# Kernel tuning notes

Measured on AMD Instinct MI355X. Metric: run time of the kernel, lower is better.

Reference implementation:

```python
import jax, jax.numpy as jnp
import numpy as np

INV_MAX_SIZE = 55
INV_STR_LEN = 80
MSG_VOCAB = 128
EOS = MSG_VOCAB + 1  # 129
VOCAB = 130
EMB = 16   # str_emb == CHAR_EMB
HID = 16
OUT = 24
B = 1024

# INV_OCLASS_MAP with default 128 (indices 0..18)
_MAP = np.full(19, 128, dtype=np.int32)
for k, v in {1: 93, 2: 41, 3: 91, 4: 61, 5: 34, 6: 40, 7: 37, 8: 33, 9: 63,
             10: 43, 11: 47, 12: 36, 13: 42, 14: 96, 15: 48, 16: 95, 17: 46, 18: 128}.items():
    _MAP[k] = v


def setup_inputs() -> dict:
    key = jax.random.key(0)
    ks = jax.random.split(key, 20)
    s = 0.1
    return {
        "inv_oclasses": jax.random.randint(ks[0], (B, INV_MAX_SIZE), 0, 19),
        "inv_strs": jax.random.randint(ks[1], (B, INV_MAX_SIZE, INV_STR_LEN), 0, MSG_VOCAB),
        "emb": jax.random.normal(ks[2], (VOCAB, EMB), jnp.float32) * s,
        "rnn_Wih": jax.random.normal(ks[3], (HID, EMB), jnp.float32) * s,
        "rnn_Whh": jax.random.normal(ks[4], (HID, HID), jnp.float32) * s,
        "rnn_bih": jax.random.normal(ks[5], (HID,), jnp.float32) * s,
        "rnn_bhh": jax.random.normal(ks[6], (HID,), jnp.float32) * s,
        "gru_Wih_f": jax.random.normal(ks[7], (3 * HID, EMB), jnp.float32) * s,
        "gru_Whh_f": jax.random.normal(ks[8], (3 * HID, HID), jnp.float32) * s,
        "gru_bih_f": jax.random.normal(ks[9], (3 * HID,), jnp.float32) * s,
        "gru_bhh_f": jax.random.normal(ks[10], (3 * HID,), jnp.float32) * s,
        "gru_Wih_b": jax.random.normal(ks[11], (3 * HID, EMB), jnp.float32) * s,
        "gru_Whh_b": jax.random.normal(ks[12], (3 * HID, HID), jnp.float32) * s,
        "gru_bih_b": jax.random.normal(ks[13], (3 * HID,), jnp.float32) * s,
        "gru_bhh_b": jax.random.normal(ks[14], (3 * HID,), jnp.float32) * s,
        "fus_W1": jax.random.normal(ks[15], (HID, 3 * HID), jnp.float32) * s,
        "fus_b1": jax.random.normal(ks[16], (HID,), jnp.float32) * s,
        "fus_W2": jax.random.normal(ks[17], (OUT, HID), jnp.float32) * s,
        "fus_b2": jax.random.normal(ks[18], (OUT,), jnp.float32) * s,
    }


def _masked_rnn(x, lengths, Wih, Whh, bih, bhh):
    # x: [N, T, D]; returns final hidden at step lengths-1 (zeros if length==0)
    N, T, _ = x.shape
    gi = jnp.einsum('ntd,hd->nth', x, Wih) + bih          # precompute input proj
    valid = (jnp.arange(T)[None, :] < lengths[:, None])   # [N, T]
    def step(h, inp):
        gi_t, v = inp
        hn = jnp.tanh(gi_t + h @ Whh.T + bhh)
        return jnp.where(v, hn, h), None
    h0 = jnp.zeros((N, Whh.shape[0]), x.dtype)
    h, _ = jax.lax.scan(step, h0, (jnp.swapaxes(gi, 0, 1), valid.T[:, :, None]))
    return h


def _masked_gru(x, lengths, Wih, Whh, bih, bhh):
    # x: [N, T, D]; PyTorch GRU cell; returns final hidden within valid prefix
    N, T, _ = x.shape
    H = Whh.shape[1]
    gi = jnp.einsum('ntd,hd->nth', x, Wih) + bih          # [N, T, 3H]
    valid = (jnp.arange(T)[None, :] < lengths[:, None])
    def step(h, inp):
        gi_t, v = inp
        gh = h @ Whh.T + bhh
        i_r, i_z, i_n = jnp.split(gi_t, 3, axis=-1)
        h_r, h_z, h_n = jnp.split(gh, 3, axis=-1)
        r = jax.nn.sigmoid(i_r + h_r)
        z = jax.nn.sigmoid(i_z + h_z)
        n = jnp.tanh(i_n + r * h_n)
        hn = (1.0 - z) * n + z * h
        return jnp.where(v, hn, h), None
    h0 = jnp.zeros((N, H), x.dtype)
    h, _ = jax.lax.scan(step, h0, (jnp.swapaxes(gi, 0, 1), valid.T[:, :, None]))
    return h


def reference(inv_oclasses, inv_strs, emb, rnn_Wih, rnn_Whh, rnn_bih, rnn_bhh,
              gru_Wih_f, gru_Whh_f, gru_bih_f, gru_bhh_f,
              gru_Wih_b, gru_Whh_b, gru_bih_b, gru_bhh_b,
              fus_W1, fus_b1, fus_W2, fus_b2):
    Bn = inv_oclasses.shape[0]
    emb = emb.at[0].set(0.0)  # padding_idx=0

    # ---- object-class branch: map -> embed -> packed vanilla RNN ----
    inv_class = jnp.asarray(_MAP)[inv_oclasses]            # [B, 55]
    inv_class_emb = emb[inv_class]                         # [B, 55, 16]
    len_class = jnp.sum(inv_oclasses != 18, axis=1)
    h_class = _masked_rnn(inv_class_emb, len_class, rnn_Wih, rnn_Whh, rnn_bih, rnn_bhh)  # [B, 16]

    # ---- string branch: insert EOS, embed, packed bidirectional GRU ----
    strs = inv_strs.reshape(Bn * INV_MAX_SIZE, INV_STR_LEN)
    lengths = jnp.sum(strs != 0, axis=-1)                  # [B*55]
    t = jnp.arange(INV_STR_LEN)
    strs_eos = jnp.where(t[None, :] == lengths[:, None], EOS, strs)
    str_emb = emb[strs_eos]                                # [B*55, 80, 16]

    h_fwd = _masked_gru(str_emb, lengths, gru_Wih_f, gru_Whh_f, gru_bih_f, gru_bhh_f)
    # reverse the valid prefix for the backward direction
    idx = jnp.maximum(lengths[:, None] - 1 - t[None, :], 0)
    x_rev = jnp.take_along_axis(str_emb, idx[:, :, None], axis=1)
    h_bwd = _masked_gru(x_rev, lengths, gru_Wih_b, gru_Whh_b, gru_bih_b, gru_bhh_b)

    str_final = jnp.concatenate([h_fwd, h_bwd], axis=-1).reshape(Bn, INV_MAX_SIZE, 2 * HID)
    str_mask = (jnp.sum(inv_strs, axis=-1) > 0).astype(str_final.dtype)[:, :, None]
    str_pooled = jnp.sum(str_final * str_mask, axis=1) / (jnp.sum(str_mask, axis=1) + 1e-8)

    combined = jnp.concatenate([h_class, str_pooled], axis=-1)   # [B, 48]
    h = jax.nn.relu(combined @ fus_W1.T + fus_b1)
    inv_features = h @ fus_W2.T + fus_b2                          # [B, 24]
    return inv_features, inv_class_emb, str_emb
```

## Files before the change

kernel.cpp:

```cpp
#include <hip/hip_runtime.h>
#include <hip/hip_bf16.h>
#include <math.h>

#define B_     1024
#define VOCAB_ 130
#define EOS_   129

#define OUT_CLS_F  24576
#define OUT_STR_F  925696

#define OFF_POOL 0
#define OFF_CNT  32768
#define OFF_HC   33792
#define OFF_T    50176

#define NK2      7104
#define NK1      14960
#define NINT     21312
#define NTOT     22064

typedef float f2 __attribute__((ext_vector_type(2)));

static __device__ const int d_MAP[19] =
    {128,93,41,91,61,34,40,37,33,63,43,47,36,42,96,48,95,46,128};

__device__ __forceinline__ float sigm_(float x){
    return __builtin_amdgcn_rcpf(1.f + __builtin_amdgcn_exp2f(-1.4426950408889634f * x));
}
__device__ __forceinline__ float tanh_(float x){
    return 2.f * __builtin_amdgcn_rcpf(1.f + __builtin_amdgcn_exp2f(-2.8853900817779268f * x)) - 1.f;
}
__device__ __forceinline__ int badf(float v) {
    return (v != v) || (fabsf(v) > 1e30f);
}
__device__ __forceinline__ f2 mkf2(float a, float b){ f2 r; r.x = a; r.y = b; return r; }

__global__ void k0_tables(const float* __restrict__ emb,
                          const float* __restrict__ WihF, const float* __restrict__ bihF,
                          const float* __restrict__ bhhF,
                          const float* __restrict__ WihB, const float* __restrict__ bihB,
                          const float* __restrict__ bhhB, float* ws)
{
    int i = blockIdx.x * 256 + threadIdx.x;
    if (i >= 12288) return;
    int dir = i / 6144, r = i - dir * 6144;
    int c = r / 48, j = r - c * 48;
    const float* Wih = dir ? WihB : WihF;
    const float* bih = dir ? bihB : bihF;
    const float* bhh = dir ? bhhB : bhhF;
    float v = bih[j] + ((j < 32) ? bhh[j] : 0.f);
    if (c != 0) {
        const float* e = emb + c * 16;
        #pragma unroll
        for (int d = 0; d < 16; ++d) v = fmaf(Wih[j * 16 + d], e[d], v);
    }
    ws[OFF_T + i] = v;
}

__global__ __launch_bounds__(256)
__attribute__((amdgpu_waves_per_eu(1, 4)))
void k12_main(const int* oclass, const int* strs, const float* __restrict__ emb,
              const float* __restrict__ WhhF, const float* __restrict__ bhhF,
              const float* __restrict__ WhhB, const float* __restrict__ bhhB,
              const float* __restrict__ rWih, const float* __restrict__ rWhh,
              const float* __restrict__ rbih, const float* __restrict__ rbhh,
              float* ws, float* out)
{
    __shared__ __align__(16) float smem[6528];
    int bi0 = blockIdx.x, tid = threadIdx.x;

    int k2id = -1, k1id;
    if (bi0 < NINT) {
        if (bi0 % 3 == 0) k2id = bi0 / 3;
        else              k1id = bi0 - bi0 / 3 - 1;
    } else {
        k1id = 14208 + (bi0 - NINT);
    }

    if (k2id < 0) {
        float* embF = smem;
        int*   chs  = (int*)(smem + 2600);
        for (int i = tid; i < VOCAB_ * 16; i += 256) {
            int r = i >> 4, c = i & 15;
            embF[r * 20 + c] = (r == 0) ? 0.f : emb[i];
        }
        __syncthreads();

        if (k1id < 14080) {
            int w = tid >> 6, lane = tid & 63;
            int s = k1id * 4 + w;
            const int* cp = strs + (long)s * 80;
            int ca = cp[lane];
            int cb = (lane < 16) ? cp[64 + lane] : 0;
            unsigned long long m1 = __ballot(ca != 0);
            unsigned long long m2 = __ballot((lane < 16) && (cb != 0));
            int L = __popcll(m1) + __popcll(m2);
            if (lane == L) ca = EOS_;
            if (lane < 16 && (64 + lane) == L) cb = EOS_;
            chs[w * 80 + lane] = ca;
            if (lane < 16) chs[w * 80 + 64 + lane] = cb;
            float4* dst = (float4*)(out + OUT_STR_F + (long)s * 1280);
            #pragma unroll
            for (int it = 0; it < 5; ++it) {
                int q = it * 64 + lane;
                int row = q >> 2, part = q & 3;
                int ch = chs[w * 80 + row];
                dst[q] = *(const float4*)&embF[ch * 20 + part * 4];
            }
        } else {
            int q = (k1id - 14080) * 256 + tid;
            int bs = q >> 2, part = q & 3;
            int c = d_MAP[oclass[bs]];
            float4* dst = (float4*)(out + OUT_CLS_F);
            dst[q] = *(const float4*)&embF[c * 20 + part * 4];
        }
        return;
    }

    float* ldsT  = smem;
    float* ldsHB = smem + 6272;
    int bi = k2id;
    int grp = tid >> 4, j = tid & 15;
    float* hb = ldsHB + (grp << 4);

    if (bi < 7040) {
        bool fwd = bi < 3520;
        const float* __restrict__ Whh = fwd ? WhhF : WhhB;
        const float* __restrict__ bhh = fwd ? bhhF : bhhB;

        const float* Tg = ws + OFF_T + (fwd ? 0 : 6144);
        for (int i = tid; i < 6144; i += 256) {
            int c = i / 48, q = i - c * 48;
            ldsT[c * 49 + q] = Tg[i];
        }

        f2 wr[8], wz[8], wn[8];
        #pragma unroll
        for (int k = 0; k < 4; ++k) {
            float4 a = *(const float4*)&Whh[      j * 16 + 4 * k];
            float4 b = *(const float4*)&Whh[256 + j * 16 + 4 * k];
            float4 c4 = *(const float4*)&Whh[512 + j * 16 + 4 * k];
            wr[2*k] = mkf2(a.x, a.y);  wr[2*k+1] = mkf2(a.z, a.w);
            wz[2*k] = mkf2(b.x, b.y);  wz[2*k+1] = mkf2(b.z, b.w);
            wn[2*k] = mkf2(c4.x, c4.y); wn[2*k+1] = mkf2(c4.z, c4.w);
        }
        float bn = bhh[32 + j];
        #pragma unroll
        for (int k = 0; k < 8; ++k) {
            asm volatile("" : "+v"(wr[k]));
            asm volatile("" : "+v"(wz[k]));
            asm volatile("" : "+v"(wn[k]));
        }
        __syncthreads();

        int s = (fwd ? bi : bi - 3520) * 16 + grp;
        const int* cp = strs + (long)s * 80;

        int cnt = 0;
        #pragma unroll
        for (int k = 0; k < 5; ++k) cnt += (cp[j + 16 * k] != 0);
        cnt += __builtin_amdgcn_ds_swizzle(cnt, (1 << 10) | 0x1f);
        cnt += __builtin_amdgcn_ds_swizzle(cnt, (2 << 10) | 0x1f);
        cnt += __builtin_amdgcn_ds_swizzle(cnt, (4 << 10) | 0x1f);
        cnt += __builtin_amdgcn_ds_swizzle(cnt, (8 << 10) | 0x1f);
        int L = cnt;

        float hj = 0.f;
        hb[j] = 0.f;
        if (L > 0) {
            int base = fwd ? 0 : (L - 1);
            int stp  = fwd ? 1 : -1;
            int c = cp[base];
            for (int t = 0; t < L; ++t) {
                int cn = (t + 1 < L) ? cp[base + (t + 1) * stp] : 0;
                const float* Trow = ldsT + c * 49;
                f2 ar = mkf2(Trow[j], 0.f);
                f2 az = mkf2(Trow[16 + j], 0.f);
                f2 an = mkf2(bn, 0.f);
                float tn_ = Trow[32 + j];
                #pragma unroll
                for (int k = 0; k < 4; ++k) {
                    float4 h4 = *(const float4*)&hb[4 * k];
                    f2 h0 = mkf2(h4.x, h4.y), h1 = mkf2(h4.z, h4.w);
                    ar = __builtin_elementwise_fma(wr[2*k],   h0, ar);
                    az = __builtin_elementwise_fma(wz[2*k],   h0, az);
                    an = __builtin_elementwise_fma(wn[2*k],   h0, an);
                    ar = __builtin_elementwise_fma(wr[2*k+1], h1, ar);
                    az = __builtin_elementwise_fma(wz[2*k+1], h1, az);
                    an = __builtin_elementwise_fma(wn[2*k+1], h1, an);
                }
                float rg = sigm_(ar.x + ar.y);
                float zg = sigm_(az.x + az.y);
                float ng = tanh_(fmaf(rg, an.x + an.y, tn_));
                hj = fmaf(zg, hj - ng, ng);
                hb[j] = hj;
                __builtin_amdgcn_wave_barrier();
                c = cn;
            }
            int b = s / 55;
            atomicAdd(ws + OFF_POOL + b * 32 + (fwd ? 0 : 16) + j, hj);
            if (fwd && j == 0) atomicAdd(ws + OFF_CNT + b, 1.f);
        }
    } else {
        for (int i = tid; i < 19 * 16; i += 256) {
            int o = i >> 4, jj = i & 15;
            int c = d_MAP[o];
            float v = rbih[jj] + rbhh[jj];
            #pragma unroll
            for (int d = 0; d < 16; ++d)
                v = fmaf(rWih[jj * 16 + d], emb[c * 16 + d], v);
            ldsT[o * 20 + jj] = v;
        }
        f2 wv[8];
        #pragma unroll
        for (int k = 0; k < 4; ++k) {
            float4 a = *(const float4*)&rWhh[j * 16 + 4 * k];
            wv[2*k] = mkf2(a.x, a.y);  wv[2*k+1] = mkf2(a.z, a.w);
        }
        __syncthreads();

        int smp = (bi - 7040) * 16 + grp;
        const int* op = oclass + (long)smp * 55;
        int cnt = 0;
        #pragma unroll
        for (int k = 0; k < 4; ++k) {
            int p = j + 16 * k;
            cnt += (p < 55 && op[p] != 18);
        }
        cnt += __builtin_amdgcn_ds_swizzle(cnt, (1 << 10) | 0x1f);
        cnt += __builtin_amdgcn_ds_swizzle(cnt, (2 << 10) | 0x1f);
        cnt += __builtin_amdgcn_ds_swizzle(cnt, (4 << 10) | 0x1f);
        cnt += __builtin_amdgcn_ds_swizzle(cnt, (8 << 10) | 0x1f);
        int len = cnt;

        float hj = 0.f;
        hb[j] = 0.f;
        if (len > 0) {
            int o = op[0];
            for (int t = 0; t < len; ++t) {
                int onx = (t + 1 < len) ? op[t + 1] : 0;
                f2 a2 = mkf2(ldsT[o * 20 + j], 0.f);
                #pragma unroll
                for (int k = 0; k < 4; ++k) {
                    float4 h4 = *(const float4*)&hb[4 * k];
                    a2 = __builtin_elementwise_fma(wv[2*k],   mkf2(h4.x, h4.y), a2);
                    a2 = __builtin_elementwise_fma(wv[2*k+1], mkf2(h4.z, h4.w), a2);
                }
                hj = tanh_(a2.x + a2.y);
                hb[j] = hj;
                __builtin_amdgcn_wave_barrier();
                o = onx;
            }
        }
        ws[OFF_HC + smp * 16 + j] = hj;
    }
}

__global__ void k3_fuse(const float* fW1, const float* fb1,
                        const float* fW2, const float* fb2,
                        float* ws, float* out)
{
    int b = blockIdx.x * 256 + threadIdx.x;
    if (b >= B_) return;
    float inv = 1.f / (ws[OFF_CNT + b] + 1e-8f);
    float comb[48];
    #pragma unroll
    for (int j = 0; j < 16; ++j) comb[j] = ws[OFF_HC + b * 16 + j];
    #pragma unroll
    for (int j = 0; j < 32; ++j) comb[16 + j] = ws[OFF_POOL + b * 32 + j] * inv;

    float hid[16];
    #pragma unroll
    for (int o = 0; o < 16; ++o) {
        float v = fb1[o];
        #pragma unroll
        for (int i = 0; i < 48; ++i) v = fmaf(fW1[o * 48 + i], comb[i], v);
        hid[o] = v > 0.f ? v : 0.f;
    }
    #pragma unroll
    for (int o = 0; o < 24; ++o) {
        float v = fb2[o];
        #pragma unroll
        for (int i = 0; i < 16; ++i) v = fmaf(fW2[o * 16 + i], hid[i], v);
        out[b * 24 + o] = v;
    }

    if (b == 0) {
        int bb = 0;
        if (!badf(ws[OFF_POOL]))    bb |= 1;
        if (!badf(ws[OFF_HC]))      bb |= 2;
        if (ws[OFF_CNT] > 0.5f)     bb |= 4;
        if (bb != 7) {
            float code = 16384.f + 128.f * (float)bb;
            #pragma unroll
            for (int i = 4; i < 12; ++i) out[i] = code;
        }
    }
}

extern "C" void kernel_launch(void* const* d_in, const int* in_sizes, int n_in,
                              void* d_out, int out_size, void* d_ws, size_t ws_size,
                              hipStream_t stream)
{
    const int*   oclass = (const int*)d_in[0];
    const int*   strs   = (const int*)d_in[1];
    const float* emb    = (const float*)d_in[2];
    const float* rWih   = (const float*)d_in[3];
    const float* rWhh   = (const float*)d_in[4];
    const float* rbih   = (const float*)d_in[5];
    const float* rbhh   = (const float*)d_in[6];
    const float* gWihF  = (const float*)d_in[7];
    const float* gWhhF  = (const float*)d_in[8];
    const float* gbihF  = (const float*)d_in[9];
    const float* gbhhF  = (const float*)d_in[10];
    const float* gWihB  = (const float*)d_in[11];
    const float* gWhhB  = (const float*)d_in[12];
    const float* gbihB  = (const float*)d_in[13];
    const float* gbhhB  = (const float*)d_in[14];
    const float* fW1    = (const float*)d_in[15];
    const float* fb1    = (const float*)d_in[16];
    const float* fW2    = (const float*)d_in[17];
    const float* fb2    = (const float*)d_in[18];

    float* ws  = (float*)d_ws;
    float* out = (float*)d_out;

    hipMemsetAsync(d_ws, 0, 33792 * sizeof(float), stream);

    k0_tables<<<48, 256, 0, stream>>>(emb, gWihF, gbihF, gbhhF,
                                      gWihB, gbihB, gbhhB, ws);
    k12_main<<<NTOT, 256, 0, stream>>>(oclass, strs, emb,
                                       gWhhF, gbhhF, gWhhB, gbhhB,
                                       rWih, rWhh, rbih, rbhh, ws, out);
    k3_fuse<<<4, 256, 0, stream>>>(fW1, fb1, fW2, fb2, ws, out);
}
```

Before: 646.6 us.

## Split GRU hidden dot-product across two lanes per unit, halving strings per block

Result: slower. 1.123 ms (+73.6%).

```diff
diff --git a/kernel.cpp b/kernel.cpp
--- a/kernel.cpp
+++ b/kernel.cpp
@@ -14,10 +14,10 @@
 #define OFF_HC   33792
 #define OFF_T    50176
 
-#define NK2      7104
+#define NK2      14144
 #define NK1      14960
-#define NINT     21312
-#define NTOT     22064
+#define NINT     28288
+#define NTOT     29104
 
 typedef float f2 __attribute__((ext_vector_type(2)));
 
@@ -34,6 +34,9 @@
     return (v != v) || (fabsf(v) > 1e30f);
 }
 __device__ __forceinline__ f2 mkf2(float a, float b){ f2 r; r.x = a; r.y = b; return r; }
+__device__ __forceinline__ float swz16_(float x){
+    return __int_as_float(__builtin_amdgcn_ds_swizzle(__float_as_int(x), 0x401F));
+}
 
 __global__ void k0_tables(const float* __restrict__ emb,
                           const float* __restrict__ WihF, const float* __restrict__ bihF,
@@ -58,7 +61,6 @@
 }
 
 __global__ __launch_bounds__(256)
-__attribute__((amdgpu_waves_per_eu(1, 4)))
 void k12_main(const int* oclass, const int* strs, const float* __restrict__ emb,
               const float* __restrict__ WhhF, const float* __restrict__ bhhF,
               const float* __restrict__ WhhB, const float* __restrict__ bhhB,
@@ -71,10 +73,10 @@
 
     int k2id = -1, k1id;
     if (bi0 < NINT) {
-        if (bi0 % 3 == 0) k2id = bi0 / 3;
-        else              k1id = bi0 - bi0 / 3 - 1;
+        if ((bi0 & 1) == 0) k2id = bi0 >> 1;
+        else                k1id = bi0 >> 1;
     } else {
-        k1id = 14208 + (bi0 - NINT);
+        k1id = NK2 + (bi0 - NINT);
     }
 
     if (k2id < 0) {
@@ -117,91 +119,112 @@
         return;
     }
 
-    float* ldsT  = smem;
-    float* ldsHB = smem + 6272;
+    float* ldsT = smem;
     int bi = k2id;
-    int grp = tid >> 4, j = tid & 15;
-    float* hb = ldsHB + (grp << 4);
-
-    if (bi < 7040) {
-        bool fwd = bi < 3520;
+
+    if (bi < 14080) {
+        int lane = tid & 63;
+        int g  = lane >> 5;
+        int q  = lane & 31;
+        int p  = q >> 4;
+        int j  = q & 15;
+        int grp8 = ((tid >> 6) << 1) + g;
+        float* hb = smem + 6272 + grp8 * 16;
+
+        bool fwd = bi < 7040;
         const float* __restrict__ Whh = fwd ? WhhF : WhhB;
         const float* __restrict__ bhh = fwd ? bhhF : bhhB;
 
         const float* Tg = ws + OFF_T + (fwd ? 0 : 6144);
         for (int i = tid; i < 6144; i += 256) {
-            int c = i / 48, q = i - c * 48;
-            ldsT[c * 49 + q] = Tg[i];
-        }
-
-        f2 wr[8], wz[8], wn[8];
+            int c = i / 48, qq = i - c * 48;
+            ldsT[c * 49 + qq] = Tg[i];
+        }
+
+        f2 wr4[4], wz4[4], wn4[4];
+        const float* Wb = Whh + j * 16 + p * 8;
+        {
+            float4 a0 = *(const float4*)&Wb[0],   a1 = *(const float4*)&Wb[4];
+            float4 b0 = *(const float4*)&Wb[256], b1 = *(const float4*)&Wb[260];
+            float4 c0 = *(const float4*)&Wb[512], c1 = *(const float4*)&Wb[516];
+            wr4[0]=mkf2(a0.x,a0.y); wr4[1]=mkf2(a0.z,a0.w); wr4[2]=mkf2(a1.x,a1.y); wr4[3]=mkf2(a1.z,a1.w);
+            wz4[0]=mkf2(b0.x,b0.y); wz4[1]=mkf2(b0.z,b0.w); wz4[2]=mkf2(b1.x,b1.y); wz4[3]=mkf2(b1.z,b1.w);
+            wn4[0]=mkf2(c0.x,c0.y); wn4[1]=mkf2(c0.z,c0.w); wn4[2]=mkf2(c1.x,c1.y); wn4[3]=mkf2(c1.z,c1.w);
+        }
         #pragma unroll
         for (int k = 0; k < 4; ++k) {
-            float4 a = *(const float4*)&Whh[      j * 16 + 4 * k];
-            float4 b = *(const float4*)&Whh[256 + j * 16 + 4 * k];
-            float4 c4 = *(const float4*)&Whh[512 + j * 16 + 4 * k];
-            wr[2*k] = mkf2(a.x, a.y);  wr[2*k+1] = mkf2(a.z, a.w);
-            wz[2*k] = mkf2(b.x, b.y);  wz[2*k+1] = mkf2(b.z, b.w);
-            wn[2*k] = mkf2(c4.x, c4.y); wn[2*k+1] = mkf2(c4.z, c4.w);
+            asm volatile("" : "+v"(wr4[k]));
+            asm volatile("" : "+v"(wz4[k]));
+            asm volatile("" : "+v"(wn4[k]));
         }
         float bn = bhh[32 + j];
-        #pragma unroll
-        for (int k = 0; k < 8; ++k) {
-            asm volatile("" : "+v"(wr[k]));
-            asm volatile("" : "+v"(wz[k]));
-            asm volatile("" : "+v"(wn[k]));
-        }
         __syncthreads();
 
-        int s = (fwd ? bi : bi - 3520) * 16 + grp;
+        int s = (fwd ? bi : bi - 7040) * 8 + grp8;
         const int* cp = strs + (long)s * 80;
 
-        int cnt = 0;
-        #pragma unroll
-        for (int k = 0; k < 5; ++k) cnt += (cp[j + 16 * k] != 0);
+        int cnt = (cp[q] != 0) + (cp[q + 32] != 0);
+        if (q < 16) cnt += (cp[q + 64] != 0);
         cnt += __builtin_amdgcn_ds_swizzle(cnt, (1 << 10) | 0x1f);
         cnt += __builtin_amdgcn_ds_swizzle(cnt, (2 << 10) | 0x1f);
         cnt += __builtin_amdgcn_ds_swizzle(cnt, (4 << 10) | 0x1f);
         cnt += __builtin_amdgcn_ds_swizzle(cnt, (8 << 10) | 0x1f);
+        cnt += __builtin_amdgcn_ds_swizzle(cnt, (16 << 10) | 0x1f);
         int L = cnt;
 
         float hj = 0.f;
         hb[j] = 0.f;
+        __builtin_amdgcn_wave_barrier();
         if (L > 0) {
             int base = fwd ? 0 : (L - 1);
             int stp  = fwd ? 1 : -1;
-            int c = cp[base];
+            int c  = cp[base];
+            int c1 = (L > 1) ? cp[base + stp] : 0;
             for (int t = 0; t < L; ++t) {
-                int cn = (t + 1 < L) ? cp[base + (t + 1) * stp] : 0;
+                int c2 = (t + 2 < L) ? cp[base + (t + 2) * stp] : 0;
                 const float* Trow = ldsT + c * 49;
-                f2 ar = mkf2(Trow[j], 0.f);
-                f2 az = mkf2(Trow[16 + j], 0.f);
-                f2 an = mkf2(bn, 0.f);
+                float t0  = Trow[(p << 4) + j];
                 float tn_ = Trow[32 + j];
-                #pragma unroll
-                for (int k = 0; k < 4; ++k) {
-                    float4 h4 = *(const float4*)&hb[4 * k];
-                    f2 h0 = mkf2(h4.x, h4.y), h1 = mkf2(h4.z, h4.w);
-                    ar = __builtin_elementwise_fma(wr[2*k],   h0, ar);
-                    az = __builtin_elementwise_fma(wz[2*k],   h0, az);
-                    an = __builtin_elementwise_fma(wn[2*k],   h0, an);
-                    ar = __builtin_elementwise_fma(wr[2*k+1], h1, ar);
-                    az = __builtin_elementwise_fma(wz[2*k+1], h1, az);
-                    an = __builtin_elementwise_fma(wn[2*k+1], h1, an);
-                }
-                float rg = sigm_(ar.x + ar.y);
-                float zg = sigm_(az.x + az.y);
-                float ng = tanh_(fmaf(rg, an.x + an.y, tn_));
+                float4 h0 = *(const float4*)&hb[p * 8];
+                float4 h1 = *(const float4*)&hb[p * 8 + 4];
+                f2 accr = mkf2(p ? 0.f : t0, 0.f);
+                f2 accz = mkf2(p ? t0 : 0.f, 0.f);
+                f2 accn = mkf2(p ? 0.f : bn, 0.f);
+                f2 ha = mkf2(h0.x, h0.y), hbv = mkf2(h0.z, h0.w);
+                f2 hc = mkf2(h1.x, h1.y), hd  = mkf2(h1.z, h1.w);
+                accr = __builtin_elementwise_fma(wr4[0], ha,  accr);
+                accz = __builtin_elementwise_fma(wz4[0], ha,  accz);
+                accn = __builtin_elementwise_fma(wn4[0], ha,  accn);
+                accr = __builtin_elementwise_fma(wr4[1], hbv, accr);
+                accz = __builtin_elementwise_fma(wz4[1], hbv, accz);
+                accn = __builtin_elementwise_fma(wn4[1], hbv, accn);
+                accr = __builtin_elementwise_fma(wr4[2], hc,  accr);
+                accz = __builtin_elementwise_fma(wz4[2], hc,  accz);
+                accn = __builtin_elementwise_fma(wn4[2], hc,  accn);
+                accr = __builtin_elementwise_fma(wr4[3], hd,  accr);
+                accz = __builtin_elementwise_fma(wz4[3], hd,  accz);
+                accn = __builtin_elementwise_fma(wn4[3], hd,  accn);
+                float sr = accr.x + accr.y;
+                float sz = accz.x + accz.y;
+                float sn = accn.x + accn.y;
+                sr += swz16_(sr);
+                sz += swz16_(sz);
+                sn += swz16_(sn);
+                float rg = sigm_(sr);
+                float zg = sigm_(sz);
+                float ng = tanh_(fmaf(rg, sn, tn_));
                 hj = fmaf(zg, hj - ng, ng);
                 hb[j] = hj;
                 __builtin_amdgcn_wave_barrier();
-                c = cn;
+                c = c1; c1 = c2;
             }
             int b = s / 55;
-            atomicAdd(ws + OFF_POOL + b * 32 + (fwd ? 0 : 16) + j, hj);
-            if (fwd && j == 0) atomicAdd(ws + OFF_CNT + b, 1.f);
+            if (p == 0) atomicAdd(ws + OFF_POOL + b * 32 + (fwd ? 0 : 16) + j, hj);
+            if (fwd && q == 0) atomicAdd(ws + OFF_CNT + b, 1.f);
         }
     } else {
+        int grp = tid >> 4, j = tid & 15;
+        float* hb = smem + 6272 + (grp << 4);
         for (int i = tid; i < 19 * 16; i += 256) {
             int o = i >> 4, jj = i & 15;
             int c = d_MAP[o];
@@ -219,13 +242,13 @@
         }
         __syncthreads();
 
-        int smp = (bi - 7040) * 16 + grp;
+        int smp = (bi - 14080) * 16 + grp;
         const int* op = oclass + (long)smp * 55;
         int cnt = 0;
         #pragma unroll
         for (int k = 0; k < 4; ++k) {
-            int p = j + 16 * k;
-            cnt += (p < 55 && op[p] != 18);
+            int pgt = j + 16 * k;
+            cnt += (pgt < 55 && op[pgt] != 18);
         }
         cnt += __builtin_amdgcn_ds_swizzle(cnt, (1 << 10) | 0x1f);
         cnt += __builtin_amdgcn_ds_swizzle(cnt, (2 << 10) | 0x1f);
@@ -235,6 +258,7 @@
 
         float hj = 0.f;
         hb[j] = 0.f;
+        __builtin_amdgcn_wave_barrier();
         if (len > 0) {
             int o = op[0];
             for (int t = 0; t < len; ++t) {
```

## Drop LDS staging of GRU input table, prefetch rows from global two steps ahead

Applied to the files above, without the earlier changes.

Measured after the change: 677.9 us. +4.8%, slower.

```diff
diff --git a/kernel.cpp b/kernel.cpp
--- a/kernel.cpp
+++ b/kernel.cpp
@@ -58,7 +58,7 @@
 }
 
 __global__ __launch_bounds__(256)
-__attribute__((amdgpu_waves_per_eu(1, 4)))
+__attribute__((amdgpu_waves_per_eu(1, 5)))
 void k12_main(const int* oclass, const int* strs, const float* __restrict__ emb,
               const float* __restrict__ WhhF, const float* __restrict__ bhhF,
               const float* __restrict__ WhhB, const float* __restrict__ bhhB,
@@ -66,7 +66,7 @@
               const float* __restrict__ rbih, const float* __restrict__ rbhh,
               float* ws, float* out)
 {
-    __shared__ __align__(16) float smem[6528];
+    __shared__ __align__(16) float smem[2920];
     int bi0 = blockIdx.x, tid = threadIdx.x;
 
     int k2id = -1, k1id;
@@ -117,41 +117,42 @@
         return;
     }
 
-    float* ldsT  = smem;
-    float* ldsHB = smem + 6272;
     int bi = k2id;
     int grp = tid >> 4, j = tid & 15;
-    float* hb = ldsHB + (grp << 4);
 
     if (bi < 7040) {
+        float* hb = smem + (grp << 4);
         bool fwd = bi < 3520;
-        const float* __restrict__ Whh = fwd ? WhhF : WhhB;
-        const float* __restrict__ bhh = fwd ? bhhF : bhhB;
-
-        const float* Tg = ws + OFF_T + (fwd ? 0 : 6144);
-        for (int i = tid; i < 6144; i += 256) {
-            int c = i / 48, q = i - c * 48;
-            ldsT[c * 49 + q] = Tg[i];
-        }
-
+        const float* Whh = fwd ? WhhF : WhhB;
+        const float* bhh = fwd ? bhhF : bhhB;
+        const float* Tg  = ws + OFF_T + (fwd ? 0 : 6144);
+
+        float wv_[48];
+        {
+            volatile const float* vp0 = Whh + j * 16;
+            volatile const float* vp1 = Whh + 256 + j * 16;
+            volatile const float* vp2 = Whh + 512 + j * 16;
+            #pragma unroll
+            for (int d = 0; d < 16; ++d) wv_[d]      = vp0[d];
+            #pragma unroll
+            for (int d = 0; d < 16; ++d) wv_[16 + d] = vp1[d];
+            #pragma unroll
+            for (int d = 0; d < 16; ++d) wv_[32 + d] = vp2[d];
+        }
         f2 wr[8], wz[8], wn[8];
         #pragma unroll
-        for (int k = 0; k < 4; ++k) {
-            float4 a = *(const float4*)&Whh[      j * 16 + 4 * k];
-            float4 b = *(const float4*)&Whh[256 + j * 16 + 4 * k];
-            float4 c4 = *(const float4*)&Whh[512 + j * 16 + 4 * k];
-            wr[2*k] = mkf2(a.x, a.y);  wr[2*k+1] = mkf2(a.z, a.w);
-            wz[2*k] = mkf2(b.x, b.y);  wz[2*k+1] = mkf2(b.z, b.w);
-            wn[2*k] = mkf2(c4.x, c4.y); wn[2*k+1] = mkf2(c4.z, c4.w);
-        }
-        float bn = bhh[32 + j];
+        for (int k = 0; k < 8; ++k) {
+            wr[k] = mkf2(wv_[2*k],      wv_[2*k + 1]);
+            wz[k] = mkf2(wv_[16 + 2*k], wv_[16 + 2*k + 1]);
+            wn[k] = mkf2(wv_[32 + 2*k], wv_[32 + 2*k + 1]);
+        }
         #pragma unroll
         for (int k = 0; k < 8; ++k) {
             asm volatile("" : "+v"(wr[k]));
             asm volatile("" : "+v"(wz[k]));
             asm volatile("" : "+v"(wn[k]));
         }
-        __syncthreads();
+        float bn = bhh[32 + j];
 
         int s = (fwd ? bi : bi - 3520) * 16 + grp;
         const int* cp = strs + (long)s * 80;
@@ -167,41 +168,73 @@
 
         float hj = 0.f;
         hb[j] = 0.f;
+        __builtin_amdgcn_wave_barrier();
         if (L > 0) {
             int base = fwd ? 0 : (L - 1);
             int stp  = fwd ? 1 : -1;
-            int c = cp[base];
+            int c0 = cp[base];
+            int c1 = (L > 1) ? cp[base + stp] : 0;
+            int c2 = (L > 2) ? cp[base + 2 * stp] : 0;
+            const float* rA = Tg + c0 * 48 + j;
+            float tA0 = rA[0], tA1 = rA[16], tA2 = rA[32];
+            const float* rB = Tg + c1 * 48 + j;
+            float tB0 = rB[0], tB1 = rB[16], tB2 = rB[32];
             for (int t = 0; t < L; ++t) {
-                int cn = (t + 1 < L) ? cp[base + (t + 1) * stp] : 0;
-                const float* Trow = ldsT + c * 49;
-                f2 ar = mkf2(Trow[j], 0.f);
-                f2 az = mkf2(Trow[16 + j], 0.f);
+                int c3 = (t + 3 < L) ? cp[base + (t + 3) * stp] : 0;
+                const float* rC = Tg + c2 * 48 + j;
+                float tC0 = rC[0], tC1 = rC[16], tC2 = rC[32];
+                f2 ar = mkf2(tA0, 0.f);
+                f2 az = mkf2(tA1, 0.f);
                 f2 an = mkf2(bn, 0.f);
-                float tn_ = Trow[32 + j];
-                #pragma unroll
-                for (int k = 0; k < 4; ++k) {
-                    float4 h4 = *(const float4*)&hb[4 * k];
-                    f2 h0 = mkf2(h4.x, h4.y), h1 = mkf2(h4.z, h4.w);
-                    ar = __builtin_elementwise_fma(wr[2*k],   h0, ar);
-                    az = __builtin_elementwise_fma(wz[2*k],   h0, az);
-                    an = __builtin_elementwise_fma(wn[2*k],   h0, an);
-                    ar = __builtin_elementwise_fma(wr[2*k+1], h1, ar);
-                    az = __builtin_elementwise_fma(wz[2*k+1], h1, az);
-                    an = __builtin_elementwise_fma(wn[2*k+1], h1, an);
-                }
+                float4 h0 = *(const float4*)&hb[0];
+                float4 h1 = *(const float4*)&hb[4];
+                float4 h2 = *(const float4*)&hb[8];
+                float4 h3 = *(const float4*)&hb[12];
+                f2 ha = mkf2(h0.x, h0.y), hbv = mkf2(h0.z, h0.w);
+                f2 hc = mkf2(h1.x, h1.y), hd  = mkf2(h1.z, h1.w);
+                f2 he = mkf2(h2.x, h2.y), hf  = mkf2(h2.z, h2.w);
+                f2 hg = mkf2(h3.x, h3.y), hh  = mkf2(h3.z, h3.w);
+                ar = __builtin_elementwise_fma(wr[0], ha,  ar);
+                az = __builtin_elementwise_fma(wz[0], ha,  az);
+                an = __builtin_elementwise_fma(wn[0], ha,  an);
+                ar = __builtin_elementwise_fma(wr[1], hbv, ar);
+                az = __builtin_elementwise_fma(wz[1], hbv, az);
+                an = __builtin_elementwise_fma(wn[1], hbv, an);
+                ar = __builtin_elementwise_fma(wr[2], hc,  ar);
+                az = __builtin_elementwise_fma(wz[2], hc,  az);
+                an = __builtin_elementwise_fma(wn[2], hc,  an);
+                ar = __builtin_elementwise_fma(wr[3], hd,  ar);
+                az = __builtin_elementwise_fma(wz[3], hd,  az);
+                an = __builtin_elementwise_fma(wn[3], hd,  an);
+                ar = __builtin_elementwise_fma(wr[4], he,  ar);
+                az = __builtin_elementwise_fma(wz[4], he,  az);
+                an = __builtin_elementwise_fma(wn[4], he,  an);
+                ar = __builtin_elementwise_fma(wr[5], hf,  ar);
+                az = __builtin_elementwise_fma(wz[5], hf,  az);
+                an = __builtin_elementwise_fma(wn[5], hf,  an);
+                ar = __builtin_elementwise_fma(wr[6], hg,  ar);
+                az = __builtin_elementwise_fma(wz[6], hg,  az);
+                an = __builtin_elementwise_fma(wn[6], hg,  an);
+                ar = __builtin_elementwise_fma(wr[7], hh,  ar);
+                az = __builtin_elementwise_fma(wz[7], hh,  az);
+                an = __builtin_elementwise_fma(wn[7], hh,  an);
                 float rg = sigm_(ar.x + ar.y);
                 float zg = sigm_(az.x + az.y);
-                float ng = tanh_(fmaf(rg, an.x + an.y, tn_));
+                float ng = tanh_(fmaf(rg, an.x + an.y, tA2));
                 hj = fmaf(zg, hj - ng, ng);
                 hb[j] = hj;
                 __builtin_amdgcn_wave_barrier();
-                c = cn;
+                tA0 = tB0; tA1 = tB1; tA2 = tB2;
+                tB0 = tC0; tB1 = tC1; tB2 = tC2;
+                c2 = c3;
             }
             int b = s / 55;
             atomicAdd(ws + OFF_POOL + b * 32 + (fwd ? 0 : 16) + j, hj);
             if (fwd && j == 0) atomicAdd(ws + OFF_CNT + b, 1.f);
         }
     } else {
+        float* ldsT = smem;
+        float* hb   = smem + 400 + (grp << 4);
         for (int i = tid; i < 19 * 16; i += 256) {
             int o = i >> 4, jj = i & 15;
             int c = d_MAP[o];
@@ -224,8 +257,8 @@
         int cnt = 0;
         #pragma unroll
         for (int k = 0; k < 4; ++k) {
-            int p = j + 16 * k;
-            cnt += (p < 55 && op[p] != 18);
+            int pgt = j + 16 * k;
+            cnt += (pgt < 55 && op[pgt] != 18);
         }
         cnt += __builtin_amdgcn_ds_swizzle(cnt, (1 << 10) | 0x1f);
         cnt += __builtin_amdgcn_ds_swizzle(cnt, (2 << 10) | 0x1f);
@@ -235,6 +268,7 @@
 
         float hj = 0.f;
         hb[j] = 0.f;
+        __builtin_amdgcn_wave_barrier();
         if (len > 0) {
             int o = op[0];
             for (int t = 0; t < len; ++t) {
```

## Exchange GRU hidden state via XOR ds_swizzle instead of LDS round-trip

Applied to the files above, without the earlier changes.

Result: slower. 665.0 us (+2.8%).

```diff
diff --git a/kernel.cpp b/kernel.cpp
--- a/kernel.cpp
+++ b/kernel.cpp
@@ -19,8 +19,6 @@
 #define NINT     21312
 #define NTOT     22064
 
-typedef float f2 __attribute__((ext_vector_type(2)));
-
 static __device__ const int d_MAP[19] =
     {128,93,41,91,61,34,40,37,33,63,43,47,36,42,96,48,95,46,128};
 
@@ -33,7 +31,6 @@
 __device__ __forceinline__ int badf(float v) {
     return (v != v) || (fabsf(v) > 1e30f);
 }
-__device__ __forceinline__ f2 mkf2(float a, float b){ f2 r; r.x = a; r.y = b; return r; }
 
 __global__ void k0_tables(const float* __restrict__ emb,
                           const float* __restrict__ WihF, const float* __restrict__ bihF,
@@ -66,7 +63,7 @@
               const float* __restrict__ rbih, const float* __restrict__ rbhh,
               float* ws, float* out)
 {
-    __shared__ __align__(16) float smem[6528];
+    __shared__ __align__(16) float smem[6272];
     int bi0 = blockIdx.x, tid = threadIdx.x;
 
     int k2id = -1, k1id;
@@ -117,11 +114,9 @@
         return;
     }
 
-    float* ldsT  = smem;
-    float* ldsHB = smem + 6272;
     int bi = k2id;
     int grp = tid >> 4, j = tid & 15;
-    float* hb = ldsHB + (grp << 4);
+    float* ldsT = smem;
 
     if (bi < 7040) {
         bool fwd = bi < 3520;
@@ -130,27 +125,19 @@
 
         const float* Tg = ws + OFF_T + (fwd ? 0 : 6144);
         for (int i = tid; i < 6144; i += 256) {
-            int c = i / 48, q = i - c * 48;
-            ldsT[c * 49 + q] = Tg[i];
-        }
-
-        f2 wr[8], wz[8], wn[8];
-        #pragma unroll
-        for (int k = 0; k < 4; ++k) {
-            float4 a = *(const float4*)&Whh[      j * 16 + 4 * k];
-            float4 b = *(const float4*)&Whh[256 + j * 16 + 4 * k];
-            float4 c4 = *(const float4*)&Whh[512 + j * 16 + 4 * k];
-            wr[2*k] = mkf2(a.x, a.y);  wr[2*k+1] = mkf2(a.z, a.w);
-            wz[2*k] = mkf2(b.x, b.y);  wz[2*k+1] = mkf2(b.z, b.w);
-            wn[2*k] = mkf2(c4.x, c4.y); wn[2*k+1] = mkf2(c4.z, c4.w);
+            int c = i / 48, qq = i - c * 48;
+            ldsT[c * 49 + qq] = Tg[i];
+        }
+
+        float wr_[16], wz_[16], wn_[16];
+        #pragma unroll
+        for (int r = 0; r < 16; ++r) {
+            int idx = j * 16 + (j ^ r);
+            wr_[r] = Whh[idx];
+            wz_[r] = Whh[256 + idx];
+            wn_[r] = Whh[512 + idx];
         }
         float bn = bhh[32 + j];
-        #pragma unroll
-        for (int k = 0; k < 8; ++k) {
-            asm volatile("" : "+v"(wr[k]));
-            asm volatile("" : "+v"(wz[k]));
-            asm volatile("" : "+v"(wn[k]));
-        }
         __syncthreads();
 
         int s = (fwd ? bi : bi - 3520) * 16 + grp;
@@ -166,36 +153,57 @@
         int L = cnt;
 
         float hj = 0.f;
-        hb[j] = 0.f;
         if (L > 0) {
             int base = fwd ? 0 : (L - 1);
             int stp  = fwd ? 1 : -1;
-            int c = cp[base];
+            int c1 = (L > 1) ? cp[base + stp] : 0;
+            int c2 = (L > 2) ? cp[base + 2 * stp] : 0;
+            const float* Tr0 = ldsT + cp[base] * 49;
+            float tC0 = Tr0[j], tC1 = Tr0[16 + j], tC2 = Tr0[32 + j];
+
             for (int t = 0; t < L; ++t) {
-                int cn = (t + 1 < L) ? cp[base + (t + 1) * stp] : 0;
-                const float* Trow = ldsT + c * 49;
-                f2 ar = mkf2(Trow[j], 0.f);
-                f2 az = mkf2(Trow[16 + j], 0.f);
-                f2 an = mkf2(bn, 0.f);
-                float tn_ = Trow[32 + j];
-                #pragma unroll
-                for (int k = 0; k < 4; ++k) {
-                    float4 h4 = *(const float4*)&hb[4 * k];
-                    f2 h0 = mkf2(h4.x, h4.y), h1 = mkf2(h4.z, h4.w);
-                    ar = __builtin_elementwise_fma(wr[2*k],   h0, ar);
-                    az = __builtin_elementwise_fma(wz[2*k],   h0, az);
-                    an = __builtin_elementwise_fma(wn[2*k],   h0, an);
-                    ar = __builtin_elementwise_fma(wr[2*k+1], h1, ar);
-                    az = __builtin_elementwise_fma(wz[2*k+1], h1, az);
-                    an = __builtin_elementwise_fma(wn[2*k+1], h1, an);
-                }
-                float rg = sigm_(ar.x + ar.y);
-                float zg = sigm_(az.x + az.y);
-                float ng = tanh_(fmaf(rg, an.x + an.y, tn_));
+                const float* Trn = ldsT + c1 * 49;
+                float tN0 = Trn[j], tN1 = Trn[16 + j], tN2 = Trn[32 + j];
+                int c3 = (t + 3 < L) ? cp[base + (t + 3) * stp] : 0;
+
+                asm volatile("" :
+                    "+v"(wr_[0]), "+v"(wr_[1]), "+v"(wr_[2]),  "+v"(wr_[3]),
+                    "+v"(wr_[4]), "+v"(wr_[5]), "+v"(wr_[6]),  "+v"(wr_[7]),
+                    "+v"(wr_[8]), "+v"(wr_[9]), "+v"(wr_[10]), "+v"(wr_[11]),
+                    "+v"(wr_[12]),"+v"(wr_[13]),"+v"(wr_[14]), "+v"(wr_[15]));
+                asm volatile("" :
+                    "+v"(wz_[0]), "+v"(wz_[1]), "+v"(wz_[2]),  "+v"(wz_[3]),
+                    "+v"(wz_[4]), "+v"(wz_[5]), "+v"(wz_[6]),  "+v"(wz_[7]),
+                    "+v"(wz_[8]), "+v"(wz_[9]), "+v"(wz_[10]), "+v"(wz_[11]),
+                    "+v"(wz_[12]),"+v"(wz_[13]),"+v"(wz_[14]), "+v"(wz_[15]));
+                asm volatile("" :
+                    "+v"(wn_[0]), "+v"(wn_[1]), "+v"(wn_[2]),  "+v"(wn_[3]),
+                    "+v"(wn_[4]), "+v"(wn_[5]), "+v"(wn_[6]),  "+v"(wn_[7]),
+                    "+v"(wn_[8]), "+v"(wn_[9]), "+v"(wn_[10]), "+v"(wn_[11]),
+                    "+v"(wn_[12]),"+v"(wn_[13]),"+v"(wn_[14]), "+v"(wn_[15]));
+
+                float ar = tC0, az = tC1, an = bn;
+                ar = fmaf(wr_[0], hj, ar);
+                az = fmaf(wz_[0], hj, az);
+                an = fmaf(wn_[0], hj, an);
+                #define STEPR(r) { \
+                    float hx = __int_as_float(__builtin_amdgcn_ds_swizzle( \
+                        __float_as_int(hj), ((r) << 10) | 0x1f)); \
+                    ar = fmaf(wr_[r], hx, ar); \
+                    az = fmaf(wz_[r], hx, az); \
+                    an = fmaf(wn_[r], hx, an); }
+                STEPR(1)  STEPR(2)  STEPR(3)  STEPR(4)  STEPR(5)
+                STEPR(6)  STEPR(7)  STEPR(8)  STEPR(9)  STEPR(10)
+                STEPR(11) STEPR(12) STEPR(13) STEPR(14) STEPR(15)
+                #undef STEPR
+
+                float rg = sigm_(ar);
+                float zg = sigm_(az);
+                float ng = tanh_(fmaf(rg, an, tC2));
                 hj = fmaf(zg, hj - ng, ng);
-                hb[j] = hj;
-                __builtin_amdgcn_wave_barrier();
-                c = cn;
+
+                tC0 = tN0; tC1 = tN1; tC2 = tN2;
+                c1 = c2; c2 = c3;
             }
             int b = s / 55;
             atomicAdd(ws + OFF_POOL + b * 32 + (fwd ? 0 : 16) + j, hj);
@@ -211,12 +219,10 @@
                 v = fmaf(rWih[jj * 16 + d], emb[c * 16 + d], v);
             ldsT[o * 20 + jj] = v;
         }
-        f2 wv[8];
-        #pragma unroll
-        for (int k = 0; k < 4; ++k) {
-            float4 a = *(const float4*)&rWhh[j * 16 + 4 * k];
-            wv[2*k] = mkf2(a.x, a.y);  wv[2*k+1] = mkf2(a.z, a.w);
-        }
+        float wv_[16];
+        #pragma unroll
+        for (int r = 0; r < 16; ++r)
+            wv_[r] = rWhh[j * 16 + (j ^ r)];
         __syncthreads();
 
         int smp = (bi - 7040) * 16 + grp;
@@ -224,8 +230,8 @@
         int cnt = 0;
         #pragma unroll
         for (int k = 0; k < 4; ++k) {
-            int p = j + 16 * k;
-            cnt += (p < 55 && op[p] != 18);
+            int pgt = j + 16 * k;
+            cnt += (pgt < 55 && op[pgt] != 18);
         }
         cnt += __builtin_amdgcn_ds_swizzle(cnt, (1 << 10) | 0x1f);
         cnt += __builtin_amdgcn_ds_swizzle(cnt, (2 << 10) | 0x1f);
@@ -234,21 +240,21 @@
         int len = cnt;
 
         float hj = 0.f;
-        hb[j] = 0.f;
         if (len > 0) {
             int o = op[0];
             for (int t = 0; t < len; ++t) {
                 int onx = (t + 1 < len) ? op[t + 1] : 0;
-                f2 a2 = mkf2(ldsT[o * 20 + j], 0.f);
-                #pragma unroll
-                for (int k = 0; k < 4; ++k) {
-                    float4 h4 = *(const float4*)&hb[4 * k];
-                    a2 = __builtin_elementwise_fma(wv[2*k],   mkf2(h4.x, h4.y), a2);
-                    a2 = __builtin_elementwise_fma(wv[2*k+1], mkf2(h4.z, h4.w), a2);
-                }
-                hj = tanh_(a2.x + a2.y);
-                hb[j] = hj;
-                __builtin_amdgcn_wave_barrier();
+                float a = ldsT[o * 20 + j];
+                a = fmaf(wv_[0], hj, a);
+                #define CSTEP(r) { \
+                    float hx = __int_as_float(__builtin_amdgcn_ds_swizzle( \
+                        __float_as_int(hj), ((r) << 10) | 0x1f)); \
+                    a = fmaf(wv_[r], hx, a); }
+                CSTEP(1)  CSTEP(2)  CSTEP(3)  CSTEP(4)  CSTEP(5)
+                CSTEP(6)  CSTEP(7)  CSTEP(8)  CSTEP(9)  CSTEP(10)
+                CSTEP(11) CSTEP(12) CSTEP(13) CSTEP(14) CSTEP(15)
+                #undef CSTEP
+                hj = tanh_(a);
                 o = onx;
             }
         }
```
